# Performance work log

Measured on AMD Instinct MI355X. Metric: run time of the kernel, lower is better.

## Reference

```python
import jax, jax.numpy as jnp
import numpy as np

# dims
BS, N, B, C, D_COL, D_PCM, EXP = 4, 512, 8, 8, 128, 32, 4
G = B * C              # 64 cortical columns
D_HID = D_COL * EXP    # 512
SURPRISE_SCALE = 1.0
EPS_LN = 1e-5
EPS_NORM = 1e-6


def _unit_normalize(x):
    return x / (jnp.linalg.norm(x, axis=-1, keepdims=True) + EPS_NORM)


def _glin(x, W, b):
    # grouped linear: x [BS,N,G,Din], W [G,Din,Dout], b [G,Dout]
    return jnp.einsum('bngi,gio->bngo', x, W) + b


def setup_inputs() -> dict:
    key = jax.random.key(0)
    ks = jax.random.split(key, 12)
    s = 0.02
    return {
        'x_col': jax.random.normal(ks[0], (BS, N, G, D_COL), jnp.float32),
        'z_hat_prev': jax.random.normal(ks[1], (BS, N, G, D_PCM), jnp.float32),
        'gamma': jnp.ones((G, D_COL), jnp.float32),
        'beta': jnp.zeros((G, D_COL), jnp.float32),
        'W_up': jax.random.normal(ks[2], (G, D_COL, D_HID), jnp.float32) * s,
        'b_up': jnp.zeros((G, D_HID), jnp.float32),
        'W_down': jax.random.normal(ks[3], (G, D_HID, D_COL), jnp.float32) * s,
        'b_down': jnp.zeros((G, D_COL), jnp.float32),
        'W_post': jax.random.normal(ks[4], (G, D_COL, 4 * D_COL + 1), jnp.float32) * s,
        'b_post': jnp.zeros((G, 4 * D_COL + 1), jnp.float32),
        'W_enc': jax.random.normal(ks[5], (G, D_COL, D_PCM), jnp.float32) * s,
        'b_enc': jnp.zeros((G, D_PCM), jnp.float32),
        'W_pred': jax.random.normal(ks[6], (G, D_PCM, D_PCM), jnp.float32) * s,
        'b_pred': jnp.zeros((G, D_PCM), jnp.float32),
        'W_gain': jnp.zeros((G, D_PCM, D_COL), jnp.float32),  # nn.init.zeros_
        'b_gain': jnp.zeros((G, D_COL), jnp.float32),
    }


def reference(x_col, z_hat_prev, gamma, beta, W_up, b_up, W_down, b_down,
              W_post, b_post, W_enc, b_enc, W_pred, b_pred, W_gain, b_gain):
    # --- PCM: encode, cross-pass surprise, gain ---
    z = _glin(x_col, W_enc, b_enc)                      # [BS,N,G,D_pcm]
    delta = z - z_hat_prev
    surprise = jnp.linalg.norm(delta, axis=-1)          # [BS,N,G]
    gain = 1.0 + 0.1 * jnp.tanh(_glin(delta, W_gain, b_gain))  # [BS,N,G,D_col]

    # --- grouped LayerNorm over D_col with per-group affine ---
    mu = jnp.mean(x_col, axis=-1, keepdims=True)
    var = jnp.mean(jnp.square(x_col - mu), axis=-1, keepdims=True)
    h = (x_col - mu) * jax.lax.rsqrt(var + EPS_LN) * gamma + beta
    h = h * gain

    # --- grouped FFN with residual ---
    h = _glin(jax.nn.gelu(_glin(h, W_up, b_up), approximate=False), W_down, b_down)
    x_out = x_col + h                                   # [BS,N,G,D_col]

    # --- PCM prediction for next pass ---
    z_hat = _glin(z, W_pred, b_pred)                    # [BS,N,G,D_pcm]

    # --- fused post projection + split ---
    proj = _glin(x_out, W_post, b_post)                 # [BS,N,G,4*D_col+1]
    proj5 = proj.reshape(BS, N, B, C, 4 * D_COL + 1)
    k_pre = proj5[..., :D_COL]
    v_post = proj5[..., D_COL:2 * D_COL]
    k_cand_raw = proj5[..., 2 * D_COL:3 * D_COL]
    v_cand = proj5[..., 3 * D_COL:4 * D_COL]
    nov_raw = proj5[..., 4 * D_COL:]

    k_cand = _unit_normalize(k_pre)
    surprise5 = surprise.reshape(BS, N, B, C)
    gate = jnp.clip(surprise5 / SURPRISE_SCALE, 0.0, 1.0)
    q_nov = _unit_normalize(k_cand_raw)
    w_nov = jax.nn.sigmoid(nov_raw[..., 0])

    return (x_out, z, z_hat, surprise, k_cand, v_post, gate, q_nov, v_cand, w_nov, surprise5)
```

## Files before the change

kernel.cpp:

```cpp
#include <hip/hip_runtime.h>

typedef unsigned short u16;
typedef __attribute__((ext_vector_type(4))) unsigned short u16x4;
typedef __attribute__((ext_vector_type(8))) short short8;
typedef __attribute__((ext_vector_type(16))) float f32x16;

#define MFMA(a,b,c) __builtin_amdgcn_mfma_f32_32x32x16_bf16((a),(b),(c),0,0,0)

static constexpr size_t OFF_XOUT = 0;
static constexpr size_t OFF_Z    = 16777216;
static constexpr size_t OFF_ZHAT = 20971520;
static constexpr size_t OFF_SUR  = 25165824;
static constexpr size_t OFF_KC   = 25296896;
static constexpr size_t OFF_VP   = 42074112;
static constexpr size_t OFF_GATE = 58851328;
static constexpr size_t OFF_QN   = 58982400;
static constexpr size_t OFF_VC   = 75759616;
static constexpr size_t OFF_WN   = 92536832;
static constexpr size_t OFF_S5   = 92667904;

static constexpr size_t WUP_T = 0;
static constexpr size_t WDN_T = 4194304;
static constexpr size_t WPO_T = 8388608;
static constexpr size_t WEN_T = 12591104;
static constexpr size_t WGN_T = 12853248;
static constexpr size_t WPR_T = 13115392;

__device__ __forceinline__ u16 f2b(float f) {
    unsigned u = __float_as_uint(f);
    unsigned r = (u + 0x7FFFu + ((u >> 16) & 1u)) >> 16;
    return (u16)r;
}
__device__ __forceinline__ float b2f(u16 b) {
    return __uint_as_float(((unsigned)b) << 16);
}
__device__ __forceinline__ int swz256(int row, int b) {
    return row * 256 + (b ^ ((row & 7) << 4) ^ (((row >> 3) & 1) << 7));
}
__device__ __forceinline__ int swz64(int row, int b) {
    return row * 64 + (b ^ ((row & 3) << 4));
}
__device__ __forceinline__ short8 fragLd256(const u16* s, int row, int ks) {
    int b = ks * 32 + ((threadIdx.x >> 5) & 1) * 16;
    return *(const short8*)((const char*)s + swz256(row, b));
}
__device__ __forceinline__ short8 fragLd64(const u16* s, int row, int ks) {
    int b = ks * 32 + ((threadIdx.x >> 5) & 1) * 16;
    return *(const short8*)((const char*)s + swz64(row, b));
}
__device__ __forceinline__ float tanh_f(float x) {
    float xc = fminf(fmaxf(x, -15.f), 15.f);
    float e = __expf(2.f * xc);
    return __fdividef(e - 1.f, e + 1.f);
}
__device__ __forceinline__ float gelu_f(float u) {
    float y = 0.7978845608f * (u + 0.044715f * u * u * u);
    return 0.5f * u * (1.f + tanh_f(y));
}

__global__ __launch_bounds__(256)
void kconv_all(const float* __restrict__ W_up, const float* __restrict__ W_down,
               const float* __restrict__ W_post, const float* __restrict__ W_enc,
               const float* __restrict__ W_gain, const float* __restrict__ W_pred,
               u16* __restrict__ ws)
{
    int b = blockIdx.x;
    const float* src; u16* dst; int K, C, bx;
    if (b < 1024)      { src = W_up;   dst = ws + WUP_T; K = 128; C = 512; bx = 8; }
    else if (b < 2048) { b -= 1024; src = W_down; dst = ws + WDN_T; K = 512; C = 128; bx = 2; }
    else if (b < 3200) { b -= 2048; src = W_post; dst = ws + WPO_T; K = 128; C = 513; bx = 9; }
    else if (b < 3328) { b -= 3200; src = W_enc;  dst = ws + WEN_T; K = 128; C = 32;  bx = 1; }
    else if (b < 3456) { b -= 3328; src = W_gain; dst = ws + WGN_T; K = 32;  C = 128; bx = 2; }
    else               { b -= 3456; src = W_pred; dst = ws + WPR_T; K = 32;  C = 32;  bx = 1; }
    const int by = (K + 63) >> 6;
    const int nb = bx * by;
    const int g = b / nb, r = b % nb;
    const int c0 = (r % bx) * 64, k0 = (r / bx) * 64;

    __shared__ float sT[64][65];
    const float* s = src + (size_t)g * K * C;
    u16* d = dst + (size_t)g * K * C;
    for (int e = threadIdx.x; e < 64 * 64; e += 256) {
        int kk = e >> 6, cc = e & 63;
        if (k0 + kk < K && c0 + cc < C)
            sT[kk][cc] = s[(size_t)(k0 + kk) * C + c0 + cc];
    }
    __syncthreads();
    for (int e = threadIdx.x; e < 64 * 64; e += 256) {
        int cc = e >> 6, kk = e & 63;
        if (k0 + kk < K && c0 + cc < C)
            d[(size_t)(c0 + cc) * K + k0 + kk] = f2b(sT[kk][cc]);
    }
}

__global__ __launch_bounds__(1024, 4)
void kfused(const float* __restrict__ x_col,
            const float* __restrict__ z_hat_prev,
            const float* __restrict__ gamma,
            const float* __restrict__ beta,
            const float* __restrict__ b_enc,
            const float* __restrict__ b_pred,
            const float* __restrict__ b_gain,
            const float* __restrict__ b_up,
            const float* __restrict__ b_down,
            const float* __restrict__ b_post,
            const u16* __restrict__ ws,
            float* __restrict__ out)
{
    const int bid = blockIdx.x;
    const int xc = bid & 7, j = bid >> 3;
    const int g = xc * 8 + (j >> 4);
    const int tile = j & 15;
    const int m0 = tile * 128;

    const int tid = threadIdx.x, lane = tid & 63;
    const int w16 = tid >> 6;
    const int wr = w16 >> 2;
    const int wc = w16 & 3;
    const int l31 = lane & 31, lh = lane >> 5;

    __shared__ u16 sX[128 * 128];
    __shared__ u16 sH[128 * 128];
    __shared__ u16 sW[128 * 128];
    __shared__ u16 sU[128 * 128];
    __shared__ float sMu[128], sRstd[128], sNrm[128], sNov[128];

    const u16* wPo = ws + WPO_T + (size_t)g * 65664;

    u16* sWe = sW;
    u16* sWg = sW + 8192;
    u16* sWp = sW + 12288;
    u16* sD  = sU;
    u16* sZ  = sU + 4096;

    for (int idx = tid; idx < 128 * 32; idx += 1024) {
        int row = idx >> 5, q = idx & 31;
        float4 v = *(const float4*)&x_col[(size_t)(m0 + row) * 8192 + g * 128 + q * 4];
        u16x4 bv; bv.x = f2b(v.x); bv.y = f2b(v.y); bv.z = f2b(v.z); bv.w = f2b(v.w);
        *(u16x4*)((char*)sX + swz256(row, q * 8)) = bv;
    }
    if (tid < 32 * 16) {
        int row = tid >> 4, slot = tid & 15;
        short8 v = *(const short8*)(ws + WEN_T + ((size_t)g * 32 + row) * 128 + slot * 8);
        *(short8*)((char*)sWe + swz256(row, slot * 16)) = v;
    }
    if (tid < 128 * 4) {
        int row = tid >> 2, slot = tid & 3;
        short8 v = *(const short8*)(ws + WGN_T + ((size_t)g * 128 + row) * 32 + slot * 8);
        *(short8*)((char*)sWg + swz64(row, slot * 16)) = v;
    }
    if (tid < 128) {
        int row = tid >> 2, slot = tid & 3;
        short8 v = *(const short8*)(ws + WPR_T + ((size_t)g * 32 + row) * 32 + slot * 8);
        *(short8*)((char*)sWp + swz64(row, slot * 16)) = v;
        sNov[tid] = b2f(wPo[(size_t)512 * 128 + tid]);
    }
    __syncthreads();

    if (w16 < 4) {
        f32x16 zacc = (f32x16)0.f;
        #pragma unroll
        for (int ks = 0; ks < 8; ++ks) {
            short8 a = fragLd256(sX, 32 * w16 + l31, ks);
            short8 b = fragLd256(sWe, l31, ks);
            zacc = MFMA(a, b, zacc);
        }
        float benc = b_enc[g * 32 + l31];
        #pragma unroll
        for (int r = 0; r < 16; ++r) {
            float zv = zacc[r] + benc;
            int row = 32 * w16 + (r & 3) + 8 * (r >> 2) + 4 * lh;
            size_t zoff = (size_t)(m0 + row) * 2048 + g * 32 + l31;
            out[OFF_Z + zoff] = zv;
            float d = zv - z_hat_prev[zoff];
            *(u16*)((char*)sD + swz64(row, l31 * 2)) = f2b(d);
            *(u16*)((char*)sZ + swz64(row, l31 * 2)) = f2b(zv);
            float ss = d * d;
            ss += __shfl_xor(ss, 1); ss += __shfl_xor(ss, 2); ss += __shfl_xor(ss, 4);
            ss += __shfl_xor(ss, 8); ss += __shfl_xor(ss, 16);
            if (l31 == 0) {
                float sur = sqrtf(ss);
                size_t p = (size_t)(m0 + row) * 64 + g;
                out[OFF_SUR + p] = sur;
                out[OFF_S5 + p] = sur;
                out[OFF_GATE + p] = fminf(fmaxf(sur, 0.f), 1.f);
            }
        }
    } else if (w16 < 8) {
        int t = tid - 256;
        int row = t >> 1, half = t & 1;
        float s1 = 0.f, s2 = 0.f;
        #pragma unroll
        for (int i = 0; i < 8; ++i) {
            short8 v = *(const short8*)((const char*)sX + swz256(row, (half * 64 + i * 8) * 2));
            #pragma unroll
            for (int jj = 0; jj < 8; ++jj) { float x = b2f((u16)v[jj]); s1 += x; s2 += x * x; }
        }
        s1 += __shfl_xor(s1, 1); s2 += __shfl_xor(s2, 1);
        if (half == 0) {
            float mu = s1 * (1.f / 128.f);
            float var = s2 * (1.f / 128.f) - mu * mu;
            sMu[row] = mu; sRstd[row] = rsqrtf(var + 1e-5f);
        }
    }
    __syncthreads();

    if (w16 < 8) {
        const int wrg = w16 >> 1;
        const int cp  = w16 & 1;
        f32x16 gacc[2];
        gacc[0] = (f32x16)0.f; gacc[1] = (f32x16)0.f;
        #pragma unroll
        for (int ks = 0; ks < 2; ++ks) {
            short8 a = fragLd64(sD, 32 * wrg + l31, ks);
            #pragma unroll
            for (int k = 0; k < 2; ++k) {
                short8 b = fragLd64(sWg, 32 * (2 * cp + k) + l31, ks);
                gacc[k] = MFMA(a, b, gacc[k]);
            }
        }
        #pragma unroll
        for (int k = 0; k < 2; ++k) {
            int col = 32 * (2 * cp + k) + l31;
            float bg = b_gain[g * 128 + col];
            float gam = gamma[g * 128 + col];
            float bet = beta[g * 128 + col];
            #pragma unroll
            for (int r = 0; r < 16; ++r) {
                int row = 32 * wrg + (r & 3) + 8 * (r >> 2) + 4 * lh;
                float gain = 1.f + 0.1f * tanh_f(gacc[k][r] + bg);
                float xv = b2f(*(const u16*)((const char*)sX + swz256(row, col * 2)));
                float h = ((xv - sMu[row]) * sRstd[row] * gam + bet) * gain;
                *(u16*)((char*)sH + swz256(row, col * 2)) = f2b(h);
            }
        }
    } else if (w16 < 12) {
        int wp = w16 - 8;
        f32x16 pacc = (f32x16)0.f;
        #pragma unroll
        for (int ks = 0; ks < 2; ++ks) {
            short8 a = fragLd64(sZ, 32 * wp + l31, ks);
            short8 b = fragLd64(sWp, l31, ks);
            pacc = MFMA(a, b, pacc);
        }
        float bpred = b_pred[g * 32 + l31];
        #pragma unroll
        for (int r = 0; r < 16; ++r) {
            int row = 32 * wp + (r & 3) + 8 * (r >> 2) + 4 * lh;
            out[OFF_ZHAT + (size_t)(m0 + row) * 2048 + g * 32 + l31] = pacc[r] + bpred;
        }
    }

    const u16* wUp = ws + WUP_T + (size_t)g * 65536;
    const u16* wDn = ws + WDN_T + (size_t)g * 65536;

    f32x16 dacc = (f32x16)0.f;

    for (int ch = 0; ch < 4; ++ch) {
        const int c0 = ch * 128;
        __syncthreads();
        for (int idx = tid; idx < 128 * 16; idx += 1024) {
            int row = idx >> 4, slot = idx & 15;
            short8 v = *(const short8*)(wUp + (size_t)(c0 + row) * 128 + slot * 8);
            *(short8*)((char*)sW + swz256(row, slot * 16)) = v;
        }
        __syncthreads();

        f32x16 uacc = (f32x16)0.f;
        #pragma unroll
        for (int ks = 0; ks < 8; ++ks) {
            short8 a = fragLd256(sH, 32 * wr + l31, ks);
            short8 b = fragLd256(sW, 32 * wc + l31, ks);
            uacc = MFMA(a, b, uacc);
        }
        {
            float bup = b_up[(size_t)g * 512 + c0 + 32 * wc + l31];
            int colB = (32 * wc + l31) * 2;
            #pragma unroll
            for (int r = 0; r < 16; ++r) {
                int row = 32 * wr + (r & 3) + 8 * (r >> 2) + 4 * lh;
                float gel = gelu_f(uacc[r] + bup);
                *(u16*)((char*)sU + swz256(row, colB)) = f2b(gel);
            }
        }
        __syncthreads();
        for (int idx = tid; idx < 128 * 16; idx += 1024) {
            int row = idx >> 4, slot = idx & 15;
            short8 v = *(const short8*)(wDn + (size_t)row * 512 + c0 + slot * 8);
            *(short8*)((char*)sW + swz256(row, slot * 16)) = v;
        }
        __syncthreads();
        #pragma unroll
        for (int ks = 0; ks < 8; ++ks) {
            short8 a = fragLd256(sU, 32 * wr + l31, ks);
            short8 b = fragLd256(sW, 32 * wc + l31, ks);
            dacc = MFMA(a, b, dacc);
        }
    }

    {
        int jc = 32 * wc + l31;
        float bd = b_down[g * 128 + jc];
        #pragma unroll
        for (int r = 0; r < 16; ++r) {
            int row = 32 * wr + (r & 3) + 8 * (r >> 2) + 4 * lh;
            size_t base = (size_t)(m0 + row) * 8192 + g * 128 + jc;
            float xo = b2f(*(const u16*)((const char*)sX + swz256(row, jc * 2)))
                       + bd + dacc[r];
            out[OFF_XOUT + base] = xo;
            *(u16*)((char*)sH + swz256(row, jc * 2)) = f2b(xo);
        }
    }

    for (int s = 0; s < 4; ++s) {
        __syncthreads();
        for (int idx = tid; idx < 128 * 16; idx += 1024) {
            int row = idx >> 4, slot = idx & 15;
            short8 v = *(const short8*)(wPo + (size_t)(s * 128 + row) * 128 + slot * 8);
            *(short8*)((char*)sW + swz256(row, slot * 16)) = v;
        }
        __syncthreads();

        f32x16 acc = (f32x16)0.f;
        #pragma unroll
        for (int ks = 0; ks < 8; ++ks) {
            short8 a = fragLd256(sH, 32 * wr + l31, ks);
            short8 b = fragLd256(sW, 32 * wc + l31, ks);
            acc = MFMA(a, b, acc);
        }
        {
            float bp = b_post[g * 513 + s * 128 + 32 * wc + l31];
            int colB = (32 * wc + l31) * 2;
            #pragma unroll
            for (int r = 0; r < 16; ++r) {
                int row = 32 * wr + (r & 3) + 8 * (r >> 2) + 4 * lh;
                *(u16*)((char*)sU + swz256(row, colB)) = f2b(acc[r] + bp);
            }
        }
        __syncthreads();

        const bool nrm = (s == 0 || s == 2);
        if (nrm) {
            int row = tid >> 3, part = tid & 7;
            float ss = 0.f;
            #pragma unroll
            for (int i = 0; i < 2; ++i) {
                short8 v = *(const short8*)((const char*)sU + swz256(row, (part * 16 + i * 8) * 2));
                #pragma unroll
                for (int jj = 0; jj < 8; ++jj) { float x = b2f((u16)v[jj]); ss += x * x; }
            }
            ss += __shfl_xor(ss, 1); ss += __shfl_xor(ss, 2); ss += __shfl_xor(ss, 4);
            if (part == 0) sNrm[row] = sqrtf(ss);
            __syncthreads();
        }
        size_t off = (s == 0) ? OFF_KC : (s == 1) ? OFF_VP : (s == 2) ? OFF_QN : OFF_VC;
        for (int idx = tid; idx < 128 * 16; idx += 1024) {
            int row = idx >> 4, slot = idx & 15;
            float inv = nrm ? __fdividef(1.f, sNrm[row] + 1e-6f) : 1.f;
            short8 v = *(const short8*)((const char*)sU + swz256(row, slot * 16));
            float4 o0, o1;
            o0.x = b2f((u16)v[0]) * inv; o0.y = b2f((u16)v[1]) * inv;
            o0.z = b2f((u16)v[2]) * inv; o0.w = b2f((u16)v[3]) * inv;
            o1.x = b2f((u16)v[4]) * inv; o1.y = b2f((u16)v[5]) * inv;
            o1.z = b2f((u16)v[6]) * inv; o1.w = b2f((u16)v[7]) * inv;
            size_t base = off + (size_t)(m0 + row) * 8192 + g * 128 + slot * 8;
            *(float4*)&out[base] = o0;
            *(float4*)&out[base + 4] = o1;
        }
    }
    __syncthreads();

    {
        int row = tid >> 3, part = tid & 7;
        float accn = 0.f;
        #pragma unroll
        for (int i = 0; i < 2; ++i) {
            short8 v = *(const short8*)((const char*)sH + swz256(row, (part * 16 + i * 8) * 2));
            #pragma unroll
            for (int jj = 0; jj < 8; ++jj) accn += b2f((u16)v[jj]) * sNov[part * 16 + i * 8 + jj];
        }
        accn += __shfl_xor(accn, 1); accn += __shfl_xor(accn, 2); accn += __shfl_xor(accn, 4);
        if (part == 0) {
            float nv = accn + b_post[g * 513 + 512];
            out[OFF_WN + (size_t)(m0 + row) * 64 + g] = __fdividef(1.f, 1.f + __expf(-nv));
        }
    }
}

extern "C" void kernel_launch(void* const* d_in, const int* in_sizes, int n_in,
                              void* d_out, int out_size, void* d_ws, size_t ws_size,
                              hipStream_t stream) {
    const float* x_col      = (const float*)d_in[0];
    const float* z_hat_prev = (const float*)d_in[1];
    const float* gamma      = (const float*)d_in[2];
    const float* beta       = (const float*)d_in[3];
    const float* W_up       = (const float*)d_in[4];
    const float* b_up       = (const float*)d_in[5];
    const float* W_down     = (const float*)d_in[6];
    const float* b_down     = (const float*)d_in[7];
    const float* W_post     = (const float*)d_in[8];
    const float* b_post     = (const float*)d_in[9];
    const float* W_enc      = (const float*)d_in[10];
    const float* b_enc      = (const float*)d_in[11];
    const float* W_pred     = (const float*)d_in[12];
    const float* b_pred     = (const float*)d_in[13];
    const float* W_gain     = (const float*)d_in[14];
    const float* b_gain     = (const float*)d_in[15];
    float* out = (float*)d_out;
    u16* ws = (u16*)d_ws;

    kconv_all<<<3520, 256, 0, stream>>>(W_up, W_down, W_post, W_enc, W_gain, W_pred, ws);
    kfused<<<1024, 1024, 0, stream>>>(x_col, z_hat_prev, gamma, beta,
                                      b_enc, b_pred, b_gain, b_up, b_down, b_post,
                                      ws, out);
}
```

Baseline: 334.1 us.

## Halve row tile to 64, merge X/H shared buffers, write post outputs from registers

The fused kernel now handles 64-row tiles with 512-thread blocks over twice as many blocks. Merging sX and sH into one buffer and shrinking sU cuts shared memory per block, which is meant to let more blocks share a CU. The residual x is kept in fp32 registers instead of re-reading the bf16 copy, and the post-projection outputs are written straight from MFMA accumulators, with row norms reduced by shuffles, instead of staging through shared memory. The cost is that each block reloads the full per-group weights for half as many rows, doubling weight traffic, and the direct per-lane stores are narrower than the previous float4 writes.

```diff
diff --git a/kernel.cpp b/kernel.cpp
--- a/kernel.cpp
+++ b/kernel.cpp
@@ -93,7 +93,7 @@
     }
 }
 
-__global__ __launch_bounds__(1024, 4)
+__global__ __launch_bounds__(512, 4)
 void kfused(const float* __restrict__ x_col,
             const float* __restrict__ z_hat_prev,
             const float* __restrict__ gamma,
@@ -109,42 +109,52 @@
 {
     const int bid = blockIdx.x;
     const int xc = bid & 7, j = bid >> 3;
-    const int g = xc * 8 + (j >> 4);
-    const int tile = j & 15;
-    const int m0 = tile * 128;
+    const int g = xc * 8 + (j >> 5);
+    const int tile = j & 31;
+    const int m0 = tile * 64;
 
     const int tid = threadIdx.x, lane = tid & 63;
-    const int w16 = tid >> 6;
-    const int wr = w16 >> 2;
-    const int wc = w16 & 3;
+    const int w8 = tid >> 6;
+    const int wr = w8 >> 2;
+    const int wc = w8 & 3;
     const int l31 = lane & 31, lh = lane >> 5;
 
-    __shared__ u16 sX[128 * 128];
-    __shared__ u16 sH[128 * 128];
+    __shared__ u16 sXH[64 * 128];
     __shared__ u16 sW[128 * 128];
-    __shared__ u16 sU[128 * 128];
-    __shared__ float sMu[128], sRstd[128], sNrm[128], sNov[128];
+    __shared__ u16 sU[64 * 128];
+    __shared__ float sMu[64], sRstd[64], sInv[64], sNov[128];
+    __shared__ float sNrm2[64][4];
 
     const u16* wPo = ws + WPO_T + (size_t)g * 65664;
 
     u16* sWe = sW;
-    u16* sWg = sW + 8192;
-    u16* sWp = sW + 12288;
+    u16* sWg = sW + 4096;
+    u16* sWp = sW + 8192;
     u16* sD  = sU;
-    u16* sZ  = sU + 4096;
-
-    for (int idx = tid; idx < 128 * 32; idx += 1024) {
+    u16* sZ  = sU + 2048;
+
+    float xres[16];
+    {
+        const int jc = 32 * wc + l31;
+        #pragma unroll
+        for (int r = 0; r < 16; ++r) {
+            int row = 32 * wr + (r & 3) + 8 * (r >> 2) + 4 * lh;
+            xres[r] = x_col[(size_t)(m0 + row) * 8192 + g * 128 + jc];
+        }
+    }
+
+    for (int idx = tid; idx < 64 * 32; idx += 512) {
         int row = idx >> 5, q = idx & 31;
         float4 v = *(const float4*)&x_col[(size_t)(m0 + row) * 8192 + g * 128 + q * 4];
         u16x4 bv; bv.x = f2b(v.x); bv.y = f2b(v.y); bv.z = f2b(v.z); bv.w = f2b(v.w);
-        *(u16x4*)((char*)sX + swz256(row, q * 8)) = bv;
-    }
-    if (tid < 32 * 16) {
+        *(u16x4*)((char*)sXH + swz256(row, q * 8)) = bv;
+    }
+    {
         int row = tid >> 4, slot = tid & 15;
         short8 v = *(const short8*)(ws + WEN_T + ((size_t)g * 32 + row) * 128 + slot * 8);
         *(short8*)((char*)sWe + swz256(row, slot * 16)) = v;
     }
-    if (tid < 128 * 4) {
+    {
         int row = tid >> 2, slot = tid & 3;
         short8 v = *(const short8*)(ws + WGN_T + ((size_t)g * 128 + row) * 32 + slot * 8);
         *(short8*)((char*)sWg + swz64(row, slot * 16)) = v;
@@ -157,11 +167,11 @@
     }
     __syncthreads();
 
-    if (w16 < 4) {
+    if (w8 < 2) {
         f32x16 zacc = (f32x16)0.f;
         #pragma unroll
         for (int ks = 0; ks < 8; ++ks) {
-            short8 a = fragLd256(sX, 32 * w16 + l31, ks);
+            short8 a = fragLd256(sXH, 32 * w8 + l31, ks);
             short8 b = fragLd256(sWe, l31, ks);
             zacc = MFMA(a, b, zacc);
         }
@@ -169,7 +179,7 @@
         #pragma unroll
         for (int r = 0; r < 16; ++r) {
             float zv = zacc[r] + benc;
-            int row = 32 * w16 + (r & 3) + 8 * (r >> 2) + 4 * lh;
+            int row = 32 * w8 + (r & 3) + 8 * (r >> 2) + 4 * lh;
             size_t zoff = (size_t)(m0 + row) * 2048 + g * 32 + l31;
             out[OFF_Z + zoff] = zv;
             float d = zv - z_hat_prev[zoff];
@@ -186,13 +196,13 @@
                 out[OFF_GATE + p] = fminf(fmaxf(sur, 0.f), 1.f);
             }
         }
-    } else if (w16 < 8) {
-        int t = tid - 256;
+    } else if (w8 < 4) {
+        int t = tid - 128;
         int row = t >> 1, half = t & 1;
         float s1 = 0.f, s2 = 0.f;
         #pragma unroll
         for (int i = 0; i < 8; ++i) {
-            short8 v = *(const short8*)((const char*)sX + swz256(row, (half * 64 + i * 8) * 2));
+            short8 v = *(const short8*)((const char*)sXH + swz256(row, (half * 64 + i * 8) * 2));
             #pragma unroll
             for (int jj = 0; jj < 8; ++jj) { float x = b2f((u16)v[jj]); s1 += x; s2 += x * x; }
         }
@@ -205,9 +215,9 @@
     }
     __syncthreads();
 
-    if (w16 < 8) {
-        const int wrg = w16 >> 1;
-        const int cp  = w16 & 1;
+    if (w8 < 4) {
+        const int wrg = w8 >> 1;
+        const int cp  = w8 & 1;
         f32x16 gacc[2];
         gacc[0] = (f32x16)0.f; gacc[1] = (f32x16)0.f;
         #pragma unroll
@@ -229,13 +239,13 @@
             for (int r = 0; r < 16; ++r) {
                 int row = 32 * wrg + (r & 3) + 8 * (r >> 2) + 4 * lh;
                 float gain = 1.f + 0.1f * tanh_f(gacc[k][r] + bg);
-                float xv = b2f(*(const u16*)((const char*)sX + swz256(row, col * 2)));
+                float xv = b2f(*(const u16*)((const char*)sXH + swz256(row, col * 2)));
                 float h = ((xv - sMu[row]) * sRstd[row] * gam + bet) * gain;
-                *(u16*)((char*)sH + swz256(row, col * 2)) = f2b(h);
-            }
-        }
-    } else if (w16 < 12) {
-        int wp = w16 - 8;
+                *(u16*)((char*)sXH + swz256(row, col * 2)) = f2b(h);
+            }
+        }
+    } else if (w8 < 6) {
+        int wp = w8 - 4;
         f32x16 pacc = (f32x16)0.f;
         #pragma unroll
         for (int ks = 0; ks < 2; ++ks) {
@@ -259,7 +269,7 @@
     for (int ch = 0; ch < 4; ++ch) {
         const int c0 = ch * 128;
         __syncthreads();
-        for (int idx = tid; idx < 128 * 16; idx += 1024) {
+        for (int idx = tid; idx < 128 * 16; idx += 512) {
             int row = idx >> 4, slot = idx & 15;
             short8 v = *(const short8*)(wUp + (size_t)(c0 + row) * 128 + slot * 8);
             *(short8*)((char*)sW + swz256(row, slot * 16)) = v;
@@ -269,7 +279,7 @@
         f32x16 uacc = (f32x16)0.f;
         #pragma unroll
         for (int ks = 0; ks < 8; ++ks) {
-            short8 a = fragLd256(sH, 32 * wr + l31, ks);
+            short8 a = fragLd256(sXH, 32 * wr + l31, ks);
             short8 b = fragLd256(sW, 32 * wc + l31, ks);
             uacc = MFMA(a, b, uacc);
         }
@@ -284,7 +294,7 @@
             }
         }
         __syncthreads();
-        for (int idx = tid; idx < 128 * 16; idx += 1024) {
+        for (int idx = tid; idx < 128 * 16; idx += 512) {
             int row = idx >> 4, slot = idx & 15;
             short8 v = *(const short8*)(wDn + (size_t)row * 512 + c0 + slot * 8);
             *(short8*)((char*)sW + swz256(row, slot * 16)) = v;
@@ -305,16 +315,15 @@
         for (int r = 0; r < 16; ++r) {
             int row = 32 * wr + (r & 3) + 8 * (r >> 2) + 4 * lh;
             size_t base = (size_t)(m0 + row) * 8192 + g * 128 + jc;
-            float xo = b2f(*(const u16*)((const char*)sX + swz256(row, jc * 2)))
-                       + bd + dacc[r];
+            float xo = xres[r] + bd + dacc[r];
             out[OFF_XOUT + base] = xo;
-            *(u16*)((char*)sH + swz256(row, jc * 2)) = f2b(xo);
+            *(u16*)((char*)sXH + swz256(row, jc * 2)) = f2b(xo);
         }
     }
 
     for (int s = 0; s < 4; ++s) {
         __syncthreads();
-        for (int idx = tid; idx < 128 * 16; idx += 1024) {
+        for (int idx = tid; idx < 128 * 16; idx += 512) {
             int row = idx >> 4, slot = idx & 15;
             short8 v = *(const short8*)(wPo + (size_t)(s * 128 + row) * 128 + slot * 8);
             *(short8*)((char*)sW + swz256(row, slot * 16)) = v;
@@ -324,58 +333,53 @@
         f32x16 acc = (f32x16)0.f;
         #pragma unroll
         for (int ks = 0; ks < 8; ++ks) {
-            short8 a = fragLd256(sH, 32 * wr + l31, ks);
+            short8 a = fragLd256(sXH, 32 * wr + l31, ks);
             short8 b = fragLd256(sW, 32 * wc + l31, ks);
             acc = MFMA(a, b, acc);
         }
-        {
-            float bp = b_post[g * 513 + s * 128 + 32 * wc + l31];
-            int colB = (32 * wc + l31) * 2;
+        const float bp = b_post[g * 513 + s * 128 + 32 * wc + l31];
+        const int jc = 32 * wc + l31;
+
+        if (s == 0 || s == 2) {
+            float pv[16];
+            #pragma unroll
+            for (int r = 0; r < 16; ++r) pv[r] = acc[r] + bp;
+            #pragma unroll
+            for (int r = 0; r < 16; ++r) {
+                float q = pv[r] * pv[r];
+                q += __shfl_xor(q, 1); q += __shfl_xor(q, 2); q += __shfl_xor(q, 4);
+                q += __shfl_xor(q, 8); q += __shfl_xor(q, 16);
+                if (l31 == 0)
+                    sNrm2[32 * wr + (r & 3) + 8 * (r >> 2) + 4 * lh][wc] = q;
+            }
+            __syncthreads();
+            if (tid < 64) {
+                float4 v = *(const float4*)&sNrm2[tid][0];
+                sInv[tid] = __fdividef(1.f, sqrtf(v.x + v.y + v.z + v.w) + 1e-6f);
+            }
+            __syncthreads();
+            size_t off = (s == 0) ? OFF_KC : OFF_QN;
             #pragma unroll
             for (int r = 0; r < 16; ++r) {
                 int row = 32 * wr + (r & 3) + 8 * (r >> 2) + 4 * lh;
-                *(u16*)((char*)sU + swz256(row, colB)) = f2b(acc[r] + bp);
-            }
-        }
-        __syncthreads();
-
-        const bool nrm = (s == 0 || s == 2);
-        if (nrm) {
-            int row = tid >> 3, part = tid & 7;
-            float ss = 0.f;
-            #pragma unroll
-            for (int i = 0; i < 2; ++i) {
-                short8 v = *(const short8*)((const char*)sU + swz256(row, (part * 16 + i * 8) * 2));
-                #pragma unroll
-                for (int jj = 0; jj < 8; ++jj) { float x = b2f((u16)v[jj]); ss += x * x; }
-            }
-            ss += __shfl_xor(ss, 1); ss += __shfl_xor(ss, 2); ss += __shfl_xor(ss, 4);
-            if (part == 0) sNrm[row] = sqrtf(ss);
-            __syncthreads();
-        }
-        size_t off = (s == 0) ? OFF_KC : (s == 1) ? OFF_VP : (s == 2) ? OFF_QN : OFF_VC;
-        for (int idx = tid; idx < 128 * 16; idx += 1024) {
-            int row = idx >> 4, slot = idx & 15;
-            float inv = nrm ? __fdividef(1.f, sNrm[row] + 1e-6f) : 1.f;
-            short8 v = *(const short8*)((const char*)sU + swz256(row, slot * 16));
-            float4 o0, o1;
-            o0.x = b2f((u16)v[0]) * inv; o0.y = b2f((u16)v[1]) * inv;
-            o0.z = b2f((u16)v[2]) * inv; o0.w = b2f((u16)v[3]) * inv;
-            o1.x = b2f((u16)v[4]) * inv; o1.y = b2f((u16)v[5]) * inv;
-            o1.z = b2f((u16)v[6]) * inv; o1.w = b2f((u16)v[7]) * inv;
-            size_t base = off + (size_t)(m0 + row) * 8192 + g * 128 + slot * 8;
-            *(float4*)&out[base] = o0;
-            *(float4*)&out[base + 4] = o1;
-        }
-    }
-    __syncthreads();
+                out[off + (size_t)(m0 + row) * 8192 + g * 128 + jc] = pv[r] * sInv[row];
+            }
+        } else {
+            size_t off = (s == 1) ? OFF_VP : OFF_VC;
+            #pragma unroll
+            for (int r = 0; r < 16; ++r) {
+                int row = 32 * wr + (r & 3) + 8 * (r >> 2) + 4 * lh;
+                out[off + (size_t)(m0 + row) * 8192 + g * 128 + jc] = acc[r] + bp;
+            }
+        }
+    }
 
     {
         int row = tid >> 3, part = tid & 7;
         float accn = 0.f;
         #pragma unroll
         for (int i = 0; i < 2; ++i) {
-            short8 v = *(const short8*)((const char*)sH + swz256(row, (part * 16 + i * 8) * 2));
+            short8 v = *(const short8*)((const char*)sXH + swz256(row, (part * 16 + i * 8) * 2));
             #pragma unroll
             for (int jj = 0; jj < 8; ++jj) accn += b2f((u16)v[jj]) * sNov[part * 16 + i * 8 + jj];
         }
@@ -410,7 +414,7 @@
     u16* ws = (u16*)d_ws;
 
     kconv_all<<<3520, 256, 0, stream>>>(W_up, W_down, W_post, W_enc, W_gain, W_pred, ws);
-    kfused<<<1024, 1024, 0, stream>>>(x_col, z_hat_prev, gamma, beta,
-                                      b_enc, b_pred, b_gain, b_up, b_down, b_post,
-                                      ws, out);
-}
+    kfused<<<2048, 512, 0, stream>>>(x_col, z_hat_prev, gamma, beta,
+                                     b_enc, b_pred, b_gain, b_up, b_down, b_post,
+                                     ws, out);
+}
```

Measured after the change: 465.2 us. 1.39x slower.

## Pre-swizzle weights in workspace, merge LDS buffers, and fuse post-proj norms

Applied to the files above, without the earlier changes.

The weight conversion kernel now writes weights already in the swizzled LDS tile layout, so the fused kernel can copy them with flat contiguous short8 loads instead of per-row swizzled stores. sX and sH are merged, which frees a second weight buffer. Up and down weight chunks now load together, removing two barriers per FFN chunk, and post-projection weights load two slices at a time. Residual x values stay in registers. The row norms for k/q now come from shuffle reductions on the MFMA accumulators, and v outputs are written straight from the accumulators. This trades barrier and address overhead for more register pressure, while the gain GEMM now spreads over all 16 waves.

```diff
diff --git a/kernel.cpp b/kernel.cpp
--- a/kernel.cpp
+++ b/kernel.cpp
@@ -19,12 +19,12 @@
 static constexpr size_t OFF_WN   = 92536832;
 static constexpr size_t OFF_S5   = 92667904;
 
-static constexpr size_t WUP_T = 0;
-static constexpr size_t WDN_T = 4194304;
-static constexpr size_t WPO_T = 8388608;
-static constexpr size_t WEN_T = 12591104;
-static constexpr size_t WGN_T = 12853248;
-static constexpr size_t WPR_T = 13115392;
+static constexpr size_t WUP_I = 0;
+static constexpr size_t WDN_I = 4194304;
+static constexpr size_t WPO_I = 8388608;
+static constexpr size_t WEN_I = 12591104;
+static constexpr size_t WGN_I = 12853248;
+static constexpr size_t WPR_I = 13115392;
 
 __device__ __forceinline__ u16 f2b(float f) {
     unsigned u = __float_as_uint(f);
@@ -56,6 +56,18 @@
 __device__ __forceinline__ float gelu_f(float u) {
     float y = 0.7978845608f * (u + 0.044715f * u * u * u);
     return 0.5f * u * (1.f + tanh_f(y));
+}
+
+__device__ __forceinline__ size_t mapElem(int wt, int k, int c) {
+    switch (wt) {
+    case 0: return (size_t)(c >> 7) * 16384 + (swz256(c & 127, 2 * k) >> 1);
+    case 1: return (size_t)(k >> 7) * 16384 + (swz256(c, 2 * (k & 127)) >> 1);
+    case 2: return (c == 512) ? (size_t)65536 + k
+                              : (size_t)(c >> 7) * 16384 + (swz256(c & 127, 2 * k) >> 1);
+    case 3: return (size_t)(swz256(c, 2 * k) >> 1);
+    case 4: return (size_t)(swz64(c, 2 * k) >> 1);
+    default: return (size_t)(swz64(c, 2 * k) >> 1);
+    }
 }
 
 __global__ __launch_bounds__(256)
@@ -65,13 +77,13 @@
                u16* __restrict__ ws)
 {
     int b = blockIdx.x;
-    const float* src; u16* dst; int K, C, bx;
-    if (b < 1024)      { src = W_up;   dst = ws + WUP_T; K = 128; C = 512; bx = 8; }
-    else if (b < 2048) { b -= 1024; src = W_down; dst = ws + WDN_T; K = 512; C = 128; bx = 2; }
-    else if (b < 3200) { b -= 2048; src = W_post; dst = ws + WPO_T; K = 128; C = 513; bx = 9; }
-    else if (b < 3328) { b -= 3200; src = W_enc;  dst = ws + WEN_T; K = 128; C = 32;  bx = 1; }
-    else if (b < 3456) { b -= 3328; src = W_gain; dst = ws + WGN_T; K = 32;  C = 128; bx = 2; }
-    else               { b -= 3456; src = W_pred; dst = ws + WPR_T; K = 32;  C = 32;  bx = 1; }
+    const float* src; u16* dst; int K, C, bx, wt; size_t gstride;
+    if (b < 1024)      { src = W_up;   dst = ws + WUP_I; K = 128; C = 512; bx = 8; wt = 0; gstride = 65536; }
+    else if (b < 2048) { b -= 1024; src = W_down; dst = ws + WDN_I; K = 512; C = 128; bx = 2; wt = 1; gstride = 65536; }
+    else if (b < 3200) { b -= 2048; src = W_post; dst = ws + WPO_I; K = 128; C = 513; bx = 9; wt = 2; gstride = 65664; }
+    else if (b < 3328) { b -= 3200; src = W_enc;  dst = ws + WEN_I; K = 128; C = 32;  bx = 1; wt = 3; gstride = 4096; }
+    else if (b < 3456) { b -= 3328; src = W_gain; dst = ws + WGN_I; K = 32;  C = 128; bx = 2; wt = 4; gstride = 4096; }
+    else               { b -= 3456; src = W_pred; dst = ws + WPR_I; K = 32;  C = 32;  bx = 1; wt = 5; gstride = 1024; }
     const int by = (K + 63) >> 6;
     const int nb = bx * by;
     const int g = b / nb, r = b % nb;
@@ -79,7 +91,7 @@
 
     __shared__ float sT[64][65];
     const float* s = src + (size_t)g * K * C;
-    u16* d = dst + (size_t)g * K * C;
+    u16* d = dst + (size_t)g * gstride;
     for (int e = threadIdx.x; e < 64 * 64; e += 256) {
         int kk = e >> 6, cc = e & 63;
         if (k0 + kk < K && c0 + cc < C)
@@ -88,8 +100,9 @@
     __syncthreads();
     for (int e = threadIdx.x; e < 64 * 64; e += 256) {
         int cc = e >> 6, kk = e & 63;
-        if (k0 + kk < K && c0 + cc < C)
-            d[(size_t)(c0 + cc) * K + k0 + kk] = f2b(sT[kk][cc]);
+        int k = k0 + kk, c = c0 + cc;
+        if (k < K && c < C)
+            d[mapElem(wt, k, c)] = f2b(sT[kk][cc]);
     }
 }
 
@@ -119,52 +132,45 @@
     const int wc = w16 & 3;
     const int l31 = lane & 31, lh = lane >> 5;
 
-    __shared__ u16 sX[128 * 128];
-    __shared__ u16 sH[128 * 128];
-    __shared__ u16 sW[128 * 128];
-    __shared__ u16 sU[128 * 128];
-    __shared__ float sMu[128], sRstd[128], sNrm[128], sNov[128];
-
-    const u16* wPo = ws + WPO_T + (size_t)g * 65664;
+    __shared__ u16 sXH[16384];
+    __shared__ u16 sW[16384];
+    __shared__ u16 sW2[16384];
+    __shared__ u16 sU[16384];
+    __shared__ float sMu[128], sRstd[128], sInv[128], sNov[128];
+    __shared__ float sNrm2[128][4];
 
     u16* sWe = sW;
     u16* sWg = sW + 8192;
-    u16* sWp = sW + 12288;
     u16* sD  = sU;
     u16* sZ  = sU + 4096;
+    u16* sWp = sU + 8192;
+
+    const u16* wUp = ws + WUP_I + (size_t)g * 65536;
+    const u16* wDn = ws + WDN_I + (size_t)g * 65536;
+    const u16* wPo = ws + WPO_I + (size_t)g * 65664;
 
     for (int idx = tid; idx < 128 * 32; idx += 1024) {
         int row = idx >> 5, q = idx & 31;
         float4 v = *(const float4*)&x_col[(size_t)(m0 + row) * 8192 + g * 128 + q * 4];
         u16x4 bv; bv.x = f2b(v.x); bv.y = f2b(v.y); bv.z = f2b(v.z); bv.w = f2b(v.w);
-        *(u16x4*)((char*)sX + swz256(row, q * 8)) = bv;
-    }
-    if (tid < 32 * 16) {
-        int row = tid >> 4, slot = tid & 15;
-        short8 v = *(const short8*)(ws + WEN_T + ((size_t)g * 32 + row) * 128 + slot * 8);
-        *(short8*)((char*)sWe + swz256(row, slot * 16)) = v;
-    }
-    if (tid < 128 * 4) {
-        int row = tid >> 2, slot = tid & 3;
-        short8 v = *(const short8*)(ws + WGN_T + ((size_t)g * 128 + row) * 32 + slot * 8);
-        *(short8*)((char*)sWg + swz64(row, slot * 16)) = v;
-    }
-    if (tid < 128) {
-        int row = tid >> 2, slot = tid & 3;
-        short8 v = *(const short8*)(ws + WPR_T + ((size_t)g * 32 + row) * 32 + slot * 8);
-        *(short8*)((char*)sWp + swz64(row, slot * 16)) = v;
-        sNov[tid] = b2f(wPo[(size_t)512 * 128 + tid]);
-    }
+        *(u16x4*)((char*)sXH + swz256(row, q * 8)) = bv;
+    }
+    {
+        const short8* se = (const short8*)(ws + WEN_I + (size_t)g * 4096);
+        const short8* sg = (const short8*)(ws + WGN_I + (size_t)g * 4096);
+        const short8* sp = (const short8*)(ws + WPR_I + (size_t)g * 1024);
+        if (tid < 512) ((short8*)sWe)[tid] = se[tid];
+        else           ((short8*)sWg)[tid - 512] = sg[tid - 512];
+        if (tid >= 896) ((short8*)sWp)[tid - 896] = sp[tid - 896];
+    }
+    if (tid < 128) sNov[tid] = b2f(wPo[65536 + tid]);
     __syncthreads();
 
     if (w16 < 4) {
         f32x16 zacc = (f32x16)0.f;
         #pragma unroll
-        for (int ks = 0; ks < 8; ++ks) {
-            short8 a = fragLd256(sX, 32 * w16 + l31, ks);
-            short8 b = fragLd256(sWe, l31, ks);
-            zacc = MFMA(a, b, zacc);
-        }
+        for (int ks = 0; ks < 8; ++ks)
+            zacc = MFMA(fragLd256(sXH, 32 * w16 + l31, ks), fragLd256(sWe, l31, ks), zacc);
         float benc = b_enc[g * 32 + l31];
         #pragma unroll
         for (int r = 0; r < 16; ++r) {
@@ -192,7 +198,7 @@
         float s1 = 0.f, s2 = 0.f;
         #pragma unroll
         for (int i = 0; i < 8; ++i) {
-            short8 v = *(const short8*)((const char*)sX + swz256(row, (half * 64 + i * 8) * 2));
+            short8 v = *(const short8*)((const char*)sXH + swz256(row, (half * 64 + i * 8) * 2));
             #pragma unroll
             for (int jj = 0; jj < 8; ++jj) { float x = b2f((u16)v[jj]); s1 += x; s2 += x * x; }
         }
@@ -205,97 +211,72 @@
     }
     __syncthreads();
 
-    if (w16 < 8) {
-        const int wrg = w16 >> 1;
-        const int cp  = w16 & 1;
-        f32x16 gacc[2];
-        gacc[0] = (f32x16)0.f; gacc[1] = (f32x16)0.f;
-        #pragma unroll
-        for (int ks = 0; ks < 2; ++ks) {
-            short8 a = fragLd64(sD, 32 * wrg + l31, ks);
-            #pragma unroll
-            for (int k = 0; k < 2; ++k) {
-                short8 b = fragLd64(sWg, 32 * (2 * cp + k) + l31, ks);
-                gacc[k] = MFMA(a, b, gacc[k]);
+    float xres[16];
+    {
+        f32x16 gacc = (f32x16)0.f;
+        #pragma unroll
+        for (int ks = 0; ks < 2; ++ks)
+            gacc = MFMA(fragLd64(sD, 32 * wr + l31, ks),
+                        fragLd64(sWg, 32 * wc + l31, ks), gacc);
+        int col = 32 * wc + l31;
+        float bg = b_gain[g * 128 + col];
+        float gam = gamma[g * 128 + col];
+        float bet = beta[g * 128 + col];
+        #pragma unroll
+        for (int r = 0; r < 16; ++r) {
+            int row = 32 * wr + (r & 3) + 8 * (r >> 2) + 4 * lh;
+            float xv = b2f(*(const u16*)((const char*)sXH + swz256(row, col * 2)));
+            xres[r] = xv;
+            float gain = 1.f + 0.1f * tanh_f(gacc[r] + bg);
+            float h = ((xv - sMu[row]) * sRstd[row] * gam + bet) * gain;
+            *(u16*)((char*)sXH + swz256(row, col * 2)) = f2b(h);
+        }
+    }
+
+    f32x16 dacc = (f32x16)0.f;
+
+    for (int ch = 0; ch < 4; ++ch) {
+        __syncthreads();
+        {
+            const short8* su = (const short8*)(wUp + ch * 16384);
+            const short8* sd = (const short8*)(wDn + ch * 16384);
+            ((short8*)sW)[tid]         = su[tid];
+            ((short8*)sW)[tid + 1024]  = su[tid + 1024];
+            ((short8*)sW2)[tid]        = sd[tid];
+            ((short8*)sW2)[tid + 1024] = sd[tid + 1024];
+        }
+        if (ch == 0 && w16 < 4) {
+            f32x16 pacc = (f32x16)0.f;
+            #pragma unroll
+            for (int ks = 0; ks < 2; ++ks)
+                pacc = MFMA(fragLd64(sZ, 32 * w16 + l31, ks), fragLd64(sWp, l31, ks), pacc);
+            float bpred = b_pred[g * 32 + l31];
+            #pragma unroll
+            for (int r = 0; r < 16; ++r) {
+                int row = 32 * w16 + (r & 3) + 8 * (r >> 2) + 4 * lh;
+                out[OFF_ZHAT + (size_t)(m0 + row) * 2048 + g * 32 + l31] = pacc[r] + bpred;
             }
         }
-        #pragma unroll
-        for (int k = 0; k < 2; ++k) {
-            int col = 32 * (2 * cp + k) + l31;
-            float bg = b_gain[g * 128 + col];
-            float gam = gamma[g * 128 + col];
-            float bet = beta[g * 128 + col];
-            #pragma unroll
-            for (int r = 0; r < 16; ++r) {
-                int row = 32 * wrg + (r & 3) + 8 * (r >> 2) + 4 * lh;
-                float gain = 1.f + 0.1f * tanh_f(gacc[k][r] + bg);
-                float xv = b2f(*(const u16*)((const char*)sX + swz256(row, col * 2)));
-                float h = ((xv - sMu[row]) * sRstd[row] * gam + bet) * gain;
-                *(u16*)((char*)sH + swz256(row, col * 2)) = f2b(h);
-            }
-        }
-    } else if (w16 < 12) {
-        int wp = w16 - 8;
-        f32x16 pacc = (f32x16)0.f;
-        #pragma unroll
-        for (int ks = 0; ks < 2; ++ks) {
-            short8 a = fragLd64(sZ, 32 * wp + l31, ks);
-            short8 b = fragLd64(sWp, l31, ks);
-            pacc = MFMA(a, b, pacc);
-        }
-        float bpred = b_pred[g * 32 + l31];
-        #pragma unroll
-        for (int r = 0; r < 16; ++r) {
-            int row = 32 * wp + (r & 3) + 8 * (r >> 2) + 4 * lh;
-            out[OFF_ZHAT + (size_t)(m0 + row) * 2048 + g * 32 + l31] = pacc[r] + bpred;
-        }
-    }
-
-    const u16* wUp = ws + WUP_T + (size_t)g * 65536;
-    const u16* wDn = ws + WDN_T + (size_t)g * 65536;
-
-    f32x16 dacc = (f32x16)0.f;
-
-    for (int ch = 0; ch < 4; ++ch) {
-        const int c0 = ch * 128;
         __syncthreads();
-        for (int idx = tid; idx < 128 * 16; idx += 1024) {
-            int row = idx >> 4, slot = idx & 15;
-            short8 v = *(const short8*)(wUp + (size_t)(c0 + row) * 128 + slot * 8);
-            *(short8*)((char*)sW + swz256(row, slot * 16)) = v;
-        }
-        __syncthreads();
-
         f32x16 uacc = (f32x16)0.f;
         #pragma unroll
-        for (int ks = 0; ks < 8; ++ks) {
-            short8 a = fragLd256(sH, 32 * wr + l31, ks);
-            short8 b = fragLd256(sW, 32 * wc + l31, ks);
-            uacc = MFMA(a, b, uacc);
-        }
+        for (int ks = 0; ks < 8; ++ks)
+            uacc = MFMA(fragLd256(sXH, 32 * wr + l31, ks),
+                        fragLd256(sW, 32 * wc + l31, ks), uacc);
         {
-            float bup = b_up[(size_t)g * 512 + c0 + 32 * wc + l31];
+            float bup = b_up[(size_t)g * 512 + ch * 128 + 32 * wc + l31];
             int colB = (32 * wc + l31) * 2;
             #pragma unroll
             for (int r = 0; r < 16; ++r) {
                 int row = 32 * wr + (r & 3) + 8 * (r >> 2) + 4 * lh;
-                float gel = gelu_f(uacc[r] + bup);
-                *(u16*)((char*)sU + swz256(row, colB)) = f2b(gel);
+                *(u16*)((char*)sU + swz256(row, colB)) = f2b(gelu_f(uacc[r] + bup));
             }
         }
         __syncthreads();
-        for (int idx = tid; idx < 128 * 16; idx += 1024) {
-            int row = idx >> 4, slot = idx & 15;
-            short8 v = *(const short8*)(wDn + (size_t)row * 512 + c0 + slot * 8);
-            *(short8*)((char*)sW + swz256(row, slot * 16)) = v;
-        }
-        __syncthreads();
-        #pragma unroll
-        for (int ks = 0; ks < 8; ++ks) {
-            short8 a = fragLd256(sU, 32 * wr + l31, ks);
-            short8 b = fragLd256(sW, 32 * wc + l31, ks);
-            dacc = MFMA(a, b, dacc);
-        }
+        #pragma unroll
+        for (int ks = 0; ks < 8; ++ks)
+            dacc = MFMA(fragLd256(sU, 32 * wr + l31, ks),
+                        fragLd256(sW2, 32 * wc + l31, ks), dacc);
     }
 
     {
@@ -305,77 +286,87 @@
         for (int r = 0; r < 16; ++r) {
             int row = 32 * wr + (r & 3) + 8 * (r >> 2) + 4 * lh;
             size_t base = (size_t)(m0 + row) * 8192 + g * 128 + jc;
-            float xo = b2f(*(const u16*)((const char*)sX + swz256(row, jc * 2)))
-                       + bd + dacc[r];
+            float xo = xres[r] + bd + dacc[r];
             out[OFF_XOUT + base] = xo;
-            *(u16*)((char*)sH + swz256(row, jc * 2)) = f2b(xo);
-        }
-    }
-
-    for (int s = 0; s < 4; ++s) {
+            *(u16*)((char*)sXH + swz256(row, jc * 2)) = f2b(xo);
+        }
+    }
+
+    for (int p = 0; p < 2; ++p) {
         __syncthreads();
-        for (int idx = tid; idx < 128 * 16; idx += 1024) {
-            int row = idx >> 4, slot = idx & 15;
-            short8 v = *(const short8*)(wPo + (size_t)(s * 128 + row) * 128 + slot * 8);
-            *(short8*)((char*)sW + swz256(row, slot * 16)) = v;
+        {
+            const short8* s0 = (const short8*)(wPo + (2 * p) * 16384);
+            const short8* s1 = (const short8*)(wPo + (2 * p + 1) * 16384);
+            ((short8*)sW)[tid]         = s0[tid];
+            ((short8*)sW)[tid + 1024]  = s0[tid + 1024];
+            ((short8*)sW2)[tid]        = s1[tid];
+            ((short8*)sW2)[tid + 1024] = s1[tid + 1024];
         }
         __syncthreads();
 
-        f32x16 acc = (f32x16)0.f;
-        #pragma unroll
-        for (int ks = 0; ks < 8; ++ks) {
-            short8 a = fragLd256(sH, 32 * wr + l31, ks);
-            short8 b = fragLd256(sW, 32 * wc + l31, ks);
-            acc = MFMA(a, b, acc);
-        }
-        {
-            float bp = b_post[g * 513 + s * 128 + 32 * wc + l31];
-            int colB = (32 * wc + l31) * 2;
-            #pragma unroll
-            for (int r = 0; r < 16; ++r) {
-                int row = 32 * wr + (r & 3) + 8 * (r >> 2) + 4 * lh;
-                *(u16*)((char*)sU + swz256(row, colB)) = f2b(acc[r] + bp);
+        for (int q = 0; q < 2; ++q) {
+            const int s = 2 * p + q;
+            const u16* buf = q ? sW2 : sW;
+            f32x16 acc = (f32x16)0.f;
+            #pragma unroll
+            for (int ks = 0; ks < 8; ++ks)
+                acc = MFMA(fragLd256(sXH, 32 * wr + l31, ks),
+                           fragLd256(buf, 32 * wc + l31, ks), acc);
+            const float bp = b_post[g * 513 + s * 128 + 32 * wc + l31];
+            const int jc = 32 * wc + l31;
+
+            if (q == 0) {
+                float pv[16];
+                #pragma unroll
+                for (int r = 0; r < 16; ++r) pv[r] = acc[r] + bp;
+                #pragma unroll
+                for (int r = 0; r < 16; ++r)
+                    *(u16*)((char*)sU + swz256(32 * wr + (r & 3) + 8 * (r >> 2) + 4 * lh, jc * 2)) = f2b(pv[r]);
+                #pragma unroll
+                for (int r = 0; r < 16; ++r) {
+                    float q2 = pv[r] * pv[r];
+                    q2 += __shfl_xor(q2, 1); q2 += __shfl_xor(q2, 2); q2 += __shfl_xor(q2, 4);
+                    q2 += __shfl_xor(q2, 8); q2 += __shfl_xor(q2, 16);
+                    if (l31 == 0)
+                        sNrm2[32 * wr + (r & 3) + 8 * (r >> 2) + 4 * lh][wc] = q2;
+                }
+                __syncthreads();
+                if (tid < 128) {
+                    float4 v = *(const float4*)&sNrm2[tid][0];
+                    sInv[tid] = __fdividef(1.f, sqrtf(v.x + v.y + v.z + v.w) + 1e-6f);
+                }
+                __syncthreads();
+                size_t off = (s == 0) ? OFF_KC : OFF_QN;
+                for (int idx = tid; idx < 128 * 16; idx += 1024) {
+                    int row = idx >> 4, slot = idx & 15;
+                    float inv = sInv[row];
+                    short8 v = *(const short8*)((const char*)sU + swz256(row, slot * 16));
+                    float4 o0, o1;
+                    o0.x = b2f((u16)v[0]) * inv; o0.y = b2f((u16)v[1]) * inv;
+                    o0.z = b2f((u16)v[2]) * inv; o0.w = b2f((u16)v[3]) * inv;
+                    o1.x = b2f((u16)v[4]) * inv; o1.y = b2f((u16)v[5]) * inv;
+                    o1.z = b2f((u16)v[6]) * inv; o1.w = b2f((u16)v[7]) * inv;
+                    size_t base = off + (size_t)(m0 + row) * 8192 + g * 128 + slot * 8;
+                    *(float4*)&out[base] = o0;
+                    *(float4*)&out[base + 4] = o1;
+                }
+            } else {
+                size_t off = (s == 1) ? OFF_VP : OFF_VC;
+                #pragma unroll
+                for (int r = 0; r < 16; ++r) {
+                    int row = 32 * wr + (r & 3) + 8 * (r >> 2) + 4 * lh;
+                    out[off + (size_t)(m0 + row) * 8192 + g * 128 + jc] = acc[r] + bp;
+                }
             }
         }
-        __syncthreads();
-
-        const bool nrm = (s == 0 || s == 2);
-        if (nrm) {
-            int row = tid >> 3, part = tid & 7;
-            float ss = 0.f;
-            #pragma unroll
-            for (int i = 0; i < 2; ++i) {
-                short8 v = *(const short8*)((const char*)sU + swz256(row, (part * 16 + i * 8) * 2));
-                #pragma unroll
-                for (int jj = 0; jj < 8; ++jj) { float x = b2f((u16)v[jj]); ss += x * x; }
-            }
-            ss += __shfl_xor(ss, 1); ss += __shfl_xor(ss, 2); ss += __shfl_xor(ss, 4);
-            if (part == 0) sNrm[row] = sqrtf(ss);
-            __syncthreads();
-        }
-        size_t off = (s == 0) ? OFF_KC : (s == 1) ? OFF_VP : (s == 2) ? OFF_QN : OFF_VC;
-        for (int idx = tid; idx < 128 * 16; idx += 1024) {
-            int row = idx >> 4, slot = idx & 15;
-            float inv = nrm ? __fdividef(1.f, sNrm[row] + 1e-6f) : 1.f;
-            short8 v = *(const short8*)((const char*)sU + swz256(row, slot * 16));
-            float4 o0, o1;
-            o0.x = b2f((u16)v[0]) * inv; o0.y = b2f((u16)v[1]) * inv;
-            o0.z = b2f((u16)v[2]) * inv; o0.w = b2f((u16)v[3]) * inv;
-            o1.x = b2f((u16)v[4]) * inv; o1.y = b2f((u16)v[5]) * inv;
-            o1.z = b2f((u16)v[6]) * inv; o1.w = b2f((u16)v[7]) * inv;
-            size_t base = off + (size_t)(m0 + row) * 8192 + g * 128 + slot * 8;
-            *(float4*)&out[base] = o0;
-            *(float4*)&out[base + 4] = o1;
-        }
-    }
-    __syncthreads();
+    }
 
     {
         int row = tid >> 3, part = tid & 7;
         float accn = 0.f;
         #pragma unroll
         for (int i = 0; i < 2; ++i) {
-            short8 v = *(const short8*)((const char*)sH + swz256(row, (part * 16 + i * 8) * 2));
+            short8 v = *(const short8*)((const char*)sXH + swz256(row, (part * 16 + i * 8) * 2));
             #pragma unroll
             for (int jj = 0; jj < 8; ++jj) accn += b2f((u16)v[jj]) * sNov[part * 16 + i * 8 + jj];
         }
```

Result: slower. 435.5 us (+30.4%).
